# Kernel optimization log

Hardware: AMD Instinct MI355X
Metric: run time of the kernel (lower is better)

The kernel has to match this reference:

```python
import jax, jax.numpy as jnp
import numpy as np

B, DE, T = 32, 256, 32
H, W, C = 128, 128, 128  # units == C


def setup_inputs() -> dict:
    key = jax.random.key(0)
    k1, k2, k3 = jax.random.split(key, 3)
    e = jax.random.normal(k1, (B, DE, T), dtype=jnp.float32)
    h = jax.random.normal(k2, (B, H, W, C), dtype=jnp.float32)
    Wd = jax.random.normal(k3, (DE, C), dtype=jnp.float32) * (1.0 / np.sqrt(DE))
    b = jnp.zeros((C,), dtype=jnp.float32)
    return {"e": e, "h": h, "Wd": Wd, "b": b}


def reference(e, h, Wd, b):
    # e: [B, DE, T]  -> dense over DE -> e_: [B, C, T]
    e_ = jnp.einsum('bdt,dc->bct', e, Wd) + b[None, :, None]
    Bh, Hh, Wh, Ch = h.shape
    HW = Hh * Wh
    # h NHWC -> [B, C, HW]
    h1 = h.transpose(0, 3, 1, 2).reshape(Bh, Ch, HW)
    # scores: [B, T, HW], contraction over channels
    s = jnp.einsum('bct,bcn->btn', e_, h1)
    # softmax over T (axis=1)
    beta = jax.nn.softmax(s, axis=1)
    # context: [B, C, HW]
    c = jnp.einsum('bct,btn->bcn', e_, beta)
    # -> [B, HW, C] -> NHWC
    c = c.transpose(0, 2, 1).reshape(Bh, Hh, Wh, Ch)
    return jnp.concatenate([c, h], axis=3)  # [B, H, W, 2C]
```

## Files before the change

### kernel.cpp

```cpp
#include <hip/hip_runtime.h>

typedef float v2f __attribute__((ext_vector_type(2)));

#define B_   32
#define DE_  256
#define T_   32
#define C_   128
#define HW_  16384

#define HSTRIDE 257

__device__ inline v2f vfma2(v2f a, v2f b, v2f c) {
#if __has_builtin(__builtin_elementwise_fma)
    return __builtin_elementwise_fma(a, b, c);
#else
    v2f r; r.x = fmaf(a.x, b.x, c.x); r.y = fmaf(a.y, b.y, c.y); return r;
#endif
}

__global__ __launch_bounds__(256) void dense_e_kernel(
    const float* __restrict__ e, const float* __restrict__ Wd,
    const float* __restrict__ bias, float* __restrict__ ews)
{
    __shared__ float elds[DE_ * T_];
    __shared__ float wlds[DE_ * 16];
    const int b   = blockIdx.y;
    const int cq  = blockIdx.x;
    const int tid = threadIdx.x;

    {
        const float4* erow = (const float4*)(e + ((size_t)b * DE_ + tid) * T_);
        float4* edst = (float4*)(elds + tid * T_);
        #pragma unroll
        for (int i = 0; i < 8; ++i) edst[i] = erow[i];

        const float4* wrow = (const float4*)(Wd + (size_t)tid * C_ + cq * 16);
        float4* wdst = (float4*)(wlds + tid * 16);
        #pragma unroll
        for (int i = 0; i < 4; ++i) wdst[i] = wrow[i];
    }
    __syncthreads();

    const int t  = tid & 31;
    const int c8 = tid >> 5;
    float a0 = 0.f, a1 = 0.f;
    #pragma unroll 8
    for (int d = 0; d < DE_; ++d) {
        float ev = elds[d * T_ + t];
        a0 = fmaf(ev, wlds[d * 16 + c8],     a0);
        a1 = fmaf(ev, wlds[d * 16 + 8 + c8], a1);
    }
    const int c0 = cq * 16 + c8;
    a0 += bias[c0];
    a1 += bias[c0 + 8];
    ews[((size_t)b * C_ + c0)     * T_ + t] = a0;
    ews[((size_t)b * C_ + c0 + 8) * T_ + t] = a1;
}

__global__ __launch_bounds__(128) void attn_fused_kernel(
    const float* __restrict__ h,
    const float* __restrict__ ews,
    float* __restrict__ out)
{
    __shared__ float hT[16 * HSTRIDE];
    __shared__ float es[2][16 * T_];

    const int b   = blockIdx.x >> 6;
    const int n0  = (blockIdx.x & 63) << 8;
    const int tid = threadIdx.x;
    const float* __restrict__ eb = ews + (size_t)b * (C_ * T_);
    const float* __restrict__ hb = h   + ((size_t)b * HW_ + n0) * C_;
    float* __restrict__       ob = out + ((size_t)b * HW_ + n0) * (2 * C_);

    v2f s0[16], s1[16];
    #pragma unroll
    for (int i = 0; i < 16; ++i) { s0[i] = (v2f){0.f, 0.f}; s1[i] = (v2f){0.f, 0.f}; }

    float4 hv[8];
    #pragma unroll
    for (int i = 0; i < 8; ++i) {
        const int idx = i * 128 + tid;
        hv[i] = *(const float4*)(hb + (size_t)(idx >> 2) * C_ + (idx & 3) * 4);
    }
    float4 ereg = ((const float4*)(eb))[tid];

    for (int ch = 0; ch < 8; ++ch) {
        if (ch) __syncthreads();

        #pragma unroll
        for (int i = 0; i < 8; ++i) {
            const int idx = i * 128 + tid;
            const int row = idx >> 2, c4 = idx & 3;
            float* d = hT + (c4 * 4) * HSTRIDE + row;
            d[0]           = hv[i].x;
            d[HSTRIDE]     = hv[i].y;
            d[2 * HSTRIDE] = hv[i].z;
            d[3 * HSTRIDE] = hv[i].w;
        }
        ((float4*)es[ch & 1])[tid] = ereg;
        __syncthreads();

        #pragma unroll
        for (int i = 0; i < 8; ++i) {
            const int idx = i * 128 + tid;
            const int row = idx >> 2, c4 = idx & 3;
            *(float4*)(ob + (size_t)row * (2 * C_) + C_ + ch * 16 + c4 * 4) = hv[i];
        }
        if (ch < 7) {
            #pragma unroll
            for (int i = 0; i < 8; ++i) {
                const int idx = i * 128 + tid;
                hv[i] = *(const float4*)(hb + (size_t)(idx >> 2) * C_ + (ch + 1) * 16 + (idx & 3) * 4);
            }
            ereg = ((const float4*)(eb + (ch + 1) * 16 * T_))[tid];
        }

        const float* esc = es[ch & 1];
        #pragma unroll
        for (int cl = 0; cl < 16; ++cl) {
            const float h0 = hT[cl * HSTRIDE + tid];
            const float h1 = hT[cl * HSTRIDE + 128 + tid];
            const float4* ec4 = (const float4*)(esc + cl * T_);
            const v2f h0v = {h0, h0}, h1v = {h1, h1};
            #pragma unroll
            for (int k = 0; k < 8; ++k) {
                const float4 ef = ec4[k];
                const v2f eA = {ef.x, ef.y}, eB = {ef.z, ef.w};
                s0[2 * k]     = vfma2(h0v, eA, s0[2 * k]);
                s0[2 * k + 1] = vfma2(h0v, eB, s0[2 * k + 1]);
                s1[2 * k]     = vfma2(h1v, eA, s1[2 * k]);
                s1[2 * k + 1] = vfma2(h1v, eB, s1[2 * k + 1]);
            }
        }
    }

    {
        v2f m2 = s0[0];
        #pragma unroll
        for (int i = 1; i < 16; ++i) { m2.x = fmaxf(m2.x, s0[i].x); m2.y = fmaxf(m2.y, s0[i].y); }
        const float m = fmaxf(m2.x, m2.y);
        float l = 0.f;
        #pragma unroll
        for (int i = 0; i < 16; ++i) {
            v2f p; p.x = __expf(s0[i].x - m); p.y = __expf(s0[i].y - m);
            s0[i] = p; l += p.x + p.y;
        }
        const float inv = 1.0f / l;
        #pragma unroll
        for (int i = 0; i < 16; ++i) { s0[i].x *= inv; s0[i].y *= inv; }
    }
    {
        v2f m2 = s1[0];
        #pragma unroll
        for (int i = 1; i < 16; ++i) { m2.x = fmaxf(m2.x, s1[i].x); m2.y = fmaxf(m2.y, s1[i].y); }
        const float m = fmaxf(m2.x, m2.y);
        float l = 0.f;
        #pragma unroll
        for (int i = 0; i < 16; ++i) {
            v2f p; p.x = __expf(s1[i].x - m); p.y = __expf(s1[i].y - m);
            s1[i] = p; l += p.x + p.y;
        }
        const float inv = 1.0f / l;
        #pragma unroll
        for (int i = 0; i < 16; ++i) { s1[i].x *= inv; s1[i].y *= inv; }
    }

    float4 ep0 = ((const float4*)(eb))[tid];
    float4 ep1 = ((const float4*)(eb + 16 * T_))[tid];
    __syncthreads();
    ((float4*)es[0])[tid] = ep0;
    ((float4*)es[1])[tid] = ep1;
    __syncthreads();
    float4 epn = ((const float4*)(eb + 2 * 16 * T_))[tid];

    for (int ch = 0; ch < 8; ++ch) {
        const float* esc = es[ch & 1];
        #pragma unroll
        for (int cl = 0; cl < 16; ++cl) {
            const float4* ec4 = (const float4*)(esc + cl * T_);
            v2f a0 = {0.f, 0.f}, a1 = {0.f, 0.f};
            #pragma unroll
            for (int k = 0; k < 8; ++k) {
                const float4 ef = ec4[k];
                const v2f eA = {ef.x, ef.y}, eB = {ef.z, ef.w};
                a0 = vfma2(eA, s0[2 * k], a0);
                a0 = vfma2(eB, s0[2 * k + 1], a0);
                a1 = vfma2(eA, s1[2 * k], a1);
                a1 = vfma2(eB, s1[2 * k + 1], a1);
            }
            hT[cl * HSTRIDE + tid]       = a0.x + a0.y;
            hT[cl * HSTRIDE + 128 + tid] = a1.x + a1.y;
        }
        __syncthreads();
        if (ch < 6) ((float4*)es[ch & 1])[tid] = epn;
        if (ch < 5) epn = ((const float4*)(eb + (ch + 3) * 16 * T_))[tid];
        #pragma unroll
        for (int i = 0; i < 8; ++i) {
            const int idx = i * 128 + tid;
            const int row = idx >> 2, c4 = idx & 3;
            const float* src = hT + (c4 * 4) * HSTRIDE + row;
            float4 st = { src[0], src[HSTRIDE], src[2 * HSTRIDE], src[3 * HSTRIDE] };
            *(float4*)(ob + (size_t)row * (2 * C_) + ch * 16 + c4 * 4) = st;
        }
        if (ch < 7) __syncthreads();
    }
}

extern "C" void kernel_launch(void* const* d_in, const int* in_sizes, int n_in,
                              void* d_out, int out_size, void* d_ws, size_t ws_size,
                              hipStream_t stream) {
    const float* e    = (const float*)d_in[0];
    const float* h    = (const float*)d_in[1];
    const float* Wd   = (const float*)d_in[2];
    const float* bias = (const float*)d_in[3];
    float* ews = (float*)d_ws;
    float* out = (float*)d_out;

    dense_e_kernel<<<dim3(8, 32), 256, 0, stream>>>(e, Wd, bias, ews);
    attn_fused_kernel<<<dim3(32 * (HW_ / 256)), 128, 0, stream>>>(h, ews, out);
}
```

Baseline: 836.0 us.

## Shrink attention block to one wavefront and drop all barriers

The fused attention kernel now runs with 64 threads (a single wavefront) per block, each thread owning four spatial positions instead of two, with channel chunks halved to 8 and iterated 16 times. Because the block is one wavefront, all __syncthreads calls are removed and LDS hand-offs rely on in-wave ordering. This cuts barrier overhead and LDS footprint per block, but raises register pressure (64 v2f score accumulators) and halves threads per block, which could lower occupancy or cause spills. Relying on implicit wave-level ordering without barriers may also be fragile.

Result: slower. 1.021 ms (+22.1%).

```diff
diff --git a/kernel.cpp b/kernel.cpp
--- a/kernel.cpp
+++ b/kernel.cpp
@@ -57,13 +57,13 @@
     ews[((size_t)b * C_ + c0 + 8) * T_ + t] = a1;
 }
 
-__global__ __launch_bounds__(128) void attn_fused_kernel(
+__global__ __launch_bounds__(64) void attn_fused_kernel(
     const float* __restrict__ h,
     const float* __restrict__ ews,
     float* __restrict__ out)
 {
-    __shared__ float hT[16 * HSTRIDE];
-    __shared__ float es[2][16 * T_];
+    __shared__ float hT[8 * HSTRIDE];
+    __shared__ float es[2][8 * T_];
 
     const int b   = blockIdx.x >> 6;
     const int n0  = (blockIdx.x & 63) << 8;
@@ -72,25 +72,26 @@
     const float* __restrict__ hb = h   + ((size_t)b * HW_ + n0) * C_;
     float* __restrict__       ob = out + ((size_t)b * HW_ + n0) * (2 * C_);
 
-    v2f s0[16], s1[16];
+    v2f s[4][16];
     #pragma unroll
-    for (int i = 0; i < 16; ++i) { s0[i] = (v2f){0.f, 0.f}; s1[i] = (v2f){0.f, 0.f}; }
+    for (int j = 0; j < 4; ++j)
+        #pragma unroll
+        for (int i = 0; i < 16; ++i) s[j][i] = (v2f){0.f, 0.f};
 
     float4 hv[8];
     #pragma unroll
     for (int i = 0; i < 8; ++i) {
-        const int idx = i * 128 + tid;
-        hv[i] = *(const float4*)(hb + (size_t)(idx >> 2) * C_ + (idx & 3) * 4);
+        const int idx = i * 64 + tid;
+        hv[i] = *(const float4*)(hb + (size_t)(idx >> 1) * C_ + (idx & 1) * 4);
     }
     float4 ereg = ((const float4*)(eb))[tid];
 
-    for (int ch = 0; ch < 8; ++ch) {
-        if (ch) __syncthreads();
-
+    #pragma unroll 1
+    for (int ch = 0; ch < 16; ++ch) {
         #pragma unroll
         for (int i = 0; i < 8; ++i) {
-            const int idx = i * 128 + tid;
-            const int row = idx >> 2, c4 = idx & 3;
+            const int idx = i * 64 + tid;
+            const int row = idx >> 1, c4 = idx & 1;
             float* d = hT + (c4 * 4) * HSTRIDE + row;
             d[0]           = hv[i].x;
             d[HSTRIDE]     = hv[i].y;
@@ -98,111 +99,97 @@
             d[3 * HSTRIDE] = hv[i].w;
         }
         ((float4*)es[ch & 1])[tid] = ereg;
-        __syncthreads();
 
         #pragma unroll
         for (int i = 0; i < 8; ++i) {
-            const int idx = i * 128 + tid;
-            const int row = idx >> 2, c4 = idx & 3;
-            *(float4*)(ob + (size_t)row * (2 * C_) + C_ + ch * 16 + c4 * 4) = hv[i];
-        }
-        if (ch < 7) {
+            const int idx = i * 64 + tid;
+            const int row = idx >> 1, c4 = idx & 1;
+            *(float4*)(ob + (size_t)row * (2 * C_) + C_ + ch * 8 + c4 * 4) = hv[i];
+        }
+        if (ch < 15) {
             #pragma unroll
             for (int i = 0; i < 8; ++i) {
-                const int idx = i * 128 + tid;
-                hv[i] = *(const float4*)(hb + (size_t)(idx >> 2) * C_ + (ch + 1) * 16 + (idx & 3) * 4);
-            }
-            ereg = ((const float4*)(eb + (ch + 1) * 16 * T_))[tid];
+                const int idx = i * 64 + tid;
+                hv[i] = *(const float4*)(hb + (size_t)(idx >> 1) * C_ + (ch + 1) * 8 + (idx & 1) * 4);
+            }
+            ereg = ((const float4*)(eb + (ch + 1) * 8 * T_))[tid];
         }
 
         const float* esc = es[ch & 1];
         #pragma unroll
-        for (int cl = 0; cl < 16; ++cl) {
-            const float h0 = hT[cl * HSTRIDE + tid];
-            const float h1 = hT[cl * HSTRIDE + 128 + tid];
+        for (int cl = 0; cl < 8; ++cl) {
+            v2f hrv[4];
+            #pragma unroll
+            for (int j = 0; j < 4; ++j) {
+                const float hr = hT[cl * HSTRIDE + 64 * j + tid];
+                hrv[j] = (v2f){hr, hr};
+            }
             const float4* ec4 = (const float4*)(esc + cl * T_);
-            const v2f h0v = {h0, h0}, h1v = {h1, h1};
             #pragma unroll
             for (int k = 0; k < 8; ++k) {
                 const float4 ef = ec4[k];
                 const v2f eA = {ef.x, ef.y}, eB = {ef.z, ef.w};
-                s0[2 * k]     = vfma2(h0v, eA, s0[2 * k]);
-                s0[2 * k + 1] = vfma2(h0v, eB, s0[2 * k + 1]);
-                s1[2 * k]     = vfma2(h1v, eA, s1[2 * k]);
-                s1[2 * k + 1] = vfma2(h1v, eB, s1[2 * k + 1]);
-            }
-        }
-    }
-
-    {
-        v2f m2 = s0[0];
-        #pragma unroll
-        for (int i = 1; i < 16; ++i) { m2.x = fmaxf(m2.x, s0[i].x); m2.y = fmaxf(m2.y, s0[i].y); }
+                #pragma unroll
+                for (int j = 0; j < 4; ++j) {
+                    s[j][2 * k]     = vfma2(hrv[j], eA, s[j][2 * k]);
+                    s[j][2 * k + 1] = vfma2(hrv[j], eB, s[j][2 * k + 1]);
+                }
+            }
+        }
+    }
+
+    #pragma unroll
+    for (int j = 0; j < 4; ++j) {
+        v2f m2 = s[j][0];
+        #pragma unroll
+        for (int i = 1; i < 16; ++i) { m2.x = fmaxf(m2.x, s[j][i].x); m2.y = fmaxf(m2.y, s[j][i].y); }
         const float m = fmaxf(m2.x, m2.y);
         float l = 0.f;
         #pragma unroll
         for (int i = 0; i < 16; ++i) {
-            v2f p; p.x = __expf(s0[i].x - m); p.y = __expf(s0[i].y - m);
-            s0[i] = p; l += p.x + p.y;
+            v2f p; p.x = __expf(s[j][i].x - m); p.y = __expf(s[j][i].y - m);
+            s[j][i] = p; l += p.x + p.y;
         }
         const float inv = 1.0f / l;
         #pragma unroll
-        for (int i = 0; i < 16; ++i) { s0[i].x *= inv; s0[i].y *= inv; }
-    }
-    {
-        v2f m2 = s1[0];
-        #pragma unroll
-        for (int i = 1; i < 16; ++i) { m2.x = fmaxf(m2.x, s1[i].x); m2.y = fmaxf(m2.y, s1[i].y); }
-        const float m = fmaxf(m2.x, m2.y);
-        float l = 0.f;
-        #pragma unroll
-        for (int i = 0; i < 16; ++i) {
-            v2f p; p.x = __expf(s1[i].x - m); p.y = __expf(s1[i].y - m);
-            s1[i] = p; l += p.x + p.y;
-        }
-        const float inv = 1.0f / l;
-        #pragma unroll
-        for (int i = 0; i < 16; ++i) { s1[i].x *= inv; s1[i].y *= inv; }
-    }
-
-    float4 ep0 = ((const float4*)(eb))[tid];
-    float4 ep1 = ((const float4*)(eb + 16 * T_))[tid];
-    __syncthreads();
-    ((float4*)es[0])[tid] = ep0;
-    ((float4*)es[1])[tid] = ep1;
-    __syncthreads();
-    float4 epn = ((const float4*)(eb + 2 * 16 * T_))[tid];
-
-    for (int ch = 0; ch < 8; ++ch) {
+        for (int i = 0; i < 16; ++i) { s[j][i].x *= inv; s[j][i].y *= inv; }
+    }
+
+    float4 ep = ((const float4*)(eb))[tid];
+    #pragma unroll 1
+    for (int ch = 0; ch < 16; ++ch) {
+        ((float4*)es[ch & 1])[tid] = ep;
+        if (ch < 15) ep = ((const float4*)(eb + (ch + 1) * 8 * T_))[tid];
+
         const float* esc = es[ch & 1];
         #pragma unroll
-        for (int cl = 0; cl < 16; ++cl) {
+        for (int cl = 0; cl < 8; ++cl) {
             const float4* ec4 = (const float4*)(esc + cl * T_);
-            v2f a0 = {0.f, 0.f}, a1 = {0.f, 0.f};
+            v2f a[4];
+            #pragma unroll
+            for (int j = 0; j < 4; ++j) a[j] = (v2f){0.f, 0.f};
             #pragma unroll
             for (int k = 0; k < 8; ++k) {
                 const float4 ef = ec4[k];
                 const v2f eA = {ef.x, ef.y}, eB = {ef.z, ef.w};
-                a0 = vfma2(eA, s0[2 * k], a0);
-                a0 = vfma2(eB, s0[2 * k + 1], a0);
-                a1 = vfma2(eA, s1[2 * k], a1);
-                a1 = vfma2(eB, s1[2 * k + 1], a1);
-            }
-            hT[cl * HSTRIDE + tid]       = a0.x + a0.y;
-            hT[cl * HSTRIDE + 128 + tid] = a1.x + a1.y;
-        }
-        __syncthreads();
-        if (ch < 6) ((float4*)es[ch & 1])[tid] = epn;
-        if (ch < 5) epn = ((const float4*)(eb + (ch + 3) * 16 * T_))[tid];
+                #pragma unroll
+                for (int j = 0; j < 4; ++j) {
+                    a[j] = vfma2(eA, s[j][2 * k], a[j]);
+                    a[j] = vfma2(eB, s[j][2 * k + 1], a[j]);
+                }
+            }
+            #pragma unroll
+            for (int j = 0; j < 4; ++j)
+                hT[cl * HSTRIDE + 64 * j + tid] = a[j].x + a[j].y;
+        }
         #pragma unroll
         for (int i = 0; i < 8; ++i) {
-            const int idx = i * 128 + tid;
-            const int row = idx >> 2, c4 = idx & 3;
+            const int idx = i * 64 + tid;
+            const int row = idx >> 1, c4 = idx & 1;
             const float* src = hT + (c4 * 4) * HSTRIDE + row;
             float4 st = { src[0], src[HSTRIDE], src[2 * HSTRIDE], src[3 * HSTRIDE] };
-            *(float4*)(ob + (size_t)row * (2 * C_) + ch * 16 + c4 * 4) = st;
-        }
-        if (ch < 7) __syncthreads();
+            *(float4*)(ob + (size_t)row * (2 * C_) + ch * 8 + c4 * 4) = st;
+        }
     }
 }
 
@@ -217,5 +204,5 @@
     float* out = (float*)d_out;
 
     dense_e_kernel<<<dim3(8, 32), 256, 0, stream>>>(e, Wd, bias, ews);
-    attn_fused_kernel<<<dim3(32 * (HW_ / 256)), 128, 0, stream>>>(h, ews, out);
-}
+    attn_fused_kernel<<<dim3(32 * (HW_ / 256)), 64, 0, stream>>>(h, ews, out);
+}
```
